# Kernel tuning notes

Measured on AMD Instinct MI355X. Metric: run time of the kernel, lower is better.

The kernel has to match this reference:

```python
import jax, jax.numpy as jnp
import numpy as np

B = 2048          # batch_size
W = 512           # input_window_size (token feature dim)
E = 16            # n_routed_experts
K = 2             # n_activated_experts (topk)
INTER = 1024      # moe_inter_dim
SH_INTER = 2 * 1024  # n_shared_experts * inter_dim
OUT = 128         # output_window_size
ROUTE_SCALE = 1.0


def setup_inputs() -> dict:
    key = jax.random.key(0)
    ks = jax.random.split(key, 18)
    sW = 1.0 / np.sqrt(W)
    sI = 1.0 / np.sqrt(INTER)
    sS = 1.0 / np.sqrt(SH_INTER)
    return {
        "x": jax.random.normal(ks[0], (B, W), jnp.float32),
        "task_id": 0,
        # gate: F.linear(x, weight) -> no bias used in forward
        "gate_w": jax.random.normal(ks[1], (E, W), jnp.float32) * sW,
        # routed experts, stacked over E. torch Linear: y = x @ w.T + b
        "w1": jax.random.normal(ks[2], (E, INTER, W), jnp.float32) * sW,
        "b1": jax.random.normal(ks[3], (E, INTER), jnp.float32) * sW,
        "w2": jax.random.normal(ks[4], (E, W, INTER), jnp.float32) * sI,
        "b2": jax.random.normal(ks[5], (E, W), jnp.float32) * sI,
        "w3": jax.random.normal(ks[6], (E, INTER, W), jnp.float32) * sW,
        "b3": jax.random.normal(ks[7], (E, INTER), jnp.float32) * sW,
        # shared expert (SwiGLU-like MLP on the window dim)
        "sw1": jax.random.normal(ks[8], (SH_INTER, W), jnp.float32) * sW,
        "sb1": jax.random.normal(ks[9], (SH_INTER,), jnp.float32) * sW,
        "sw2": jax.random.normal(ks[10], (W, SH_INTER), jnp.float32) * sS,
        "sb2": jax.random.normal(ks[11], (W,), jnp.float32) * sS,
        "sw3": jax.random.normal(ks[12], (SH_INTER, W), jnp.float32) * sW,
        "sb3": jax.random.normal(ks[13], (SH_INTER,), jnp.float32) * sW,
        # output layer
        "ow": jax.random.normal(ks[14], (OUT, W), jnp.float32) * sW,
        "ob": jax.random.normal(ks[15], (OUT,), jnp.float32) * sW,
    }


def reference(x, task_id, gate_w, w1, b1, w2, b2, w3, b3,
              sw1, sb1, sw2, sb2, sw3, sb3, ow, ob):
    xf = x.reshape(x.shape[0], -1)                      # [B, W]
    b = xf.shape[0]

    # --- gate: softmax scores, top-k routing weights ---
    scores = jax.nn.softmax(xf @ gate_w.T, axis=-1)     # [B, E] (fp32 softmax)
    top_w, top_i = jax.lax.top_k(scores, K)             # [B, K]
    top_w = (top_w * ROUTE_SCALE).astype(xf.dtype)
    # dense combine weights: zero except selected experts (topk indices distinct)
    combine = jnp.zeros((b, E), xf.dtype).at[jnp.arange(b)[:, None], top_i].add(top_w)

    # --- routed experts (dense, all experts on all tokens, masked combine) ---
    h1 = jnp.einsum('bw,eiw->bei', xf, w1) + b1          # [B, E, INTER]
    h3 = jnp.einsum('bw,eiw->bei', xf, w3) + b3
    h = jax.nn.leaky_relu(h1) * h3                       # leaky_relu slope 0.01
    eo = jnp.einsum('bei,ewi->bew', h, w2) + b2          # [B, E, W]
    y = jnp.einsum('bew,be->bw', eo, combine)            # weighted combine

    # --- shared expert ---
    z = (jax.nn.leaky_relu(xf @ sw1.T + sb1) * (xf @ sw3.T + sb3)) @ sw2.T + sb2

    out = (y + z) @ ow.T + ob                            # [B, OUT]
    return out.reshape(B, OUT)
```

## Files before the change

kernel.cpp:

```cpp
#include <hip/hip_runtime.h>

#define B_TOK 2048
#define W_DIM 512
#define E_N 16
#define INTER 1024
#define SH_INTER 2048
#define OUT_DIM 128

typedef unsigned short u16;
typedef unsigned int u32;
typedef __attribute__((ext_vector_type(8))) short bf16x8;
typedef __attribute__((ext_vector_type(4))) float f32x4;

#define WAITV(N) asm volatile("s_waitcnt vmcnt(" #N ")" ::: "memory")
#define WAITL()  asm volatile("s_waitcnt lgkmcnt(0)" ::: "memory")
#define SBAR()   __builtin_amdgcn_s_barrier()

__device__ __forceinline__ u16 f2b(float f) {
    union { float f; unsigned u; } x; x.f = f;
    unsigned r = x.u + 0x7FFFu + ((x.u >> 16) & 1u);
    return (u16)(r >> 16);
}

__device__ __forceinline__ u32 cvtpk(float lo, float hi) {
    u32 r;
    asm("v_cvt_pk_bf16_f32 %0, %1, %2" : "=v"(r) : "v"(lo), "v"(hi));
    return r;
}

__device__ __forceinline__ void gld16(const void* g, void* l) {
    __builtin_amdgcn_global_load_lds(
        (const __attribute__((address_space(1))) void*)g,
        (__attribute__((address_space(3))) void*)l, 16, 0, 0);
}


struct CastSeg { const float4* src; uint4* dst; int n8; };
struct CastArgs { CastSeg s[2]; };

__global__ __launch_bounds__(256)
void cast_small(CastArgs a) {
    int rem = blockIdx.x * 2048;
    int s = 0;
    while (rem >= a.s[s].n8) { rem -= a.s[s].n8; ++s; }
    const float4* __restrict__ src = a.s[s].src + (size_t)rem * 2;
    uint4* __restrict__ dst = a.s[s].dst + rem;
    const int t = threadIdx.x;
    #pragma unroll
    for (int k = 0; k < 8; ++k) {
        float4 v0 = src[(size_t)(t + k * 256) * 2];
        float4 v1 = src[(size_t)(t + k * 256) * 2 + 1];
        uint4 o;
        o.x = cvtpk(v0.x, v0.y);
        o.y = cvtpk(v0.z, v0.w);
        o.z = cvtpk(v1.x, v1.y);
        o.w = cvtpk(v1.z, v1.w);
        dst[t + k * 256] = o;
    }
}

__global__ __launch_bounds__(256)
void gate_topk(const float* __restrict__ x, const float* __restrict__ gw,
               int* __restrict__ topi, float* __restrict__ topw) {
    const int lane = threadIdx.x & 63;
    const int wv   = threadIdx.x >> 6;
    const int t    = blockIdx.x * 4 + wv;
    const int e = lane >> 2, q = lane & 3;
    const float4* xr = (const float4*)(x + (size_t)t * W_DIM);
    const float4* wr = (const float4*)(gw + (size_t)e * W_DIM);
    float s = 0.f;
    #pragma unroll
    for (int i = 0; i < W_DIM / 16; ++i) {
        float4 a = xr[q + 4 * i];
        float4 b = wr[q + 4 * i];
        s += a.x * b.x + a.y * b.y + a.z * b.z + a.w * b.w;
    }
    s += __shfl_xor(s, 1);
    s += __shfl_xor(s, 2);
    float sc[16];
    #pragma unroll
    for (int ee = 0; ee < 16; ++ee) sc[ee] = __shfl(s, ee * 4);
    float mx = sc[0];
    #pragma unroll
    for (int ee = 1; ee < 16; ++ee) mx = fmaxf(mx, sc[ee]);
    float p[16]; float sum = 0.f;
    #pragma unroll
    for (int ee = 0; ee < 16; ++ee) { p[ee] = expf(sc[ee] - mx); sum += p[ee]; }
    const float inv = 1.f / sum;
    int i0 = 0; float v0 = sc[0];
    #pragma unroll
    for (int ee = 1; ee < 16; ++ee) if (sc[ee] > v0) { v0 = sc[ee]; i0 = ee; }
    int i1 = -1; float v1 = -1e30f;
    #pragma unroll
    for (int ee = 0; ee < 16; ++ee) if (ee != i0 && sc[ee] > v1) { v1 = sc[ee]; i1 = ee; }
    if (lane == 0) {
        topi[t * 2 + 0] = i0; topi[t * 2 + 1] = i1;
        topw[t * 2 + 0] = p[i0] * inv; topw[t * 2 + 1] = p[i1] * inv;
    }
}

__global__ __launch_bounds__(256)
void route_build(const int* __restrict__ topi, const float* __restrict__ topw,
                 int* __restrict__ meta, int* __restrict__ glist,
                 float* __restrict__ job_w, int* __restrict__ t2r) {
    __shared__ int cnt[16], cur[16], offs[16];
    const int tid = threadIdx.x;
    if (tid < 16) { cnt[tid] = 0; cur[tid] = 0; }
    __syncthreads();
    for (int i = tid; i < 2 * B_TOK; i += 256) atomicAdd(&cnt[topi[i]], 1);
    __syncthreads();
    if (tid == 0) {
        int acc = 0, jc = 0;
        for (int e = 0; e < 16; ++e) {
            offs[e] = acc; meta[e] = cnt[e]; meta[32 + e] = acc; acc += cnt[e];
        }
        for (int e = 0; e < 16; ++e)
            for (int m = 0; m < cnt[e]; m += 128) { meta[64 + jc] = e; meta[128 + jc] = m; ++jc; }
        for (int m = 0; m < B_TOK; m += 128) { meta[64 + jc] = 16; meta[128 + jc] = m; ++jc; }
        meta[50] = jc;
        jc = 0;
        for (int e = 0; e < 16; ++e)
            for (int m = 0; m < cnt[e]; m += 64) { meta[192 + jc] = e; meta[304 + jc] = m; ++jc; }
        for (int m = 0; m < B_TOK; m += 64) { meta[192 + jc] = 16; meta[304 + jc] = m; ++jc; }
        meta[51] = jc;
    }
    __syncthreads();
    for (int i = tid; i < 2 * B_TOK; i += 256) {
        int e = topi[i];
        int pos = atomicAdd(&cur[e], 1);
        int row = offs[e] + pos;
        glist[row] = i >> 1;
        job_w[row] = topw[i];
        t2r[i] = row;
    }
    for (int t = tid; t < B_TOK; t += 256) glist[4096 + t] = t;
}

struct BReg { float4 a1, b1, a3, b3; };

__global__ __launch_bounds__(256)
void g1_dual(const u16* __restrict__ xb, const int* __restrict__ glist, const int* __restrict__ meta,
             const float* __restrict__ w1, const float* __restrict__ w3,
             const float* __restrict__ b1, const float* __restrict__ b3,
             const float* __restrict__ sw1, const float* __restrict__ sw3,
             const float* __restrict__ sb1, const float* __restrict__ sb3,
             u16* __restrict__ hbuf, u16* __restrict__ pbuf) {
    const int job = blockIdx.x;
    if (job >= meta[50]) return;
    const int e  = meta[64 + job];
    const int m0 = meta[128 + job];
    const bool sh = (e == 16);
    if (!sh && blockIdx.y >= (INTER / 64)) return;
    const int n0 = blockIdx.y * 64;
    const int N  = sh ? SH_INTER : INTER;
    const float* B1 = sh ? sw1 : (w1 + (size_t)e * INTER * W_DIM);
    const float* B3 = sh ? sw3 : (w3 + (size_t)e * INTER * W_DIM);
    const float* bb1 = sh ? sb1 : (b1 + (size_t)e * INTER);
    const float* bb3 = sh ? sb3 : (b3 + (size_t)e * INTER);
    const int abase = sh ? (4096 + m0) : (meta[32 + e] + m0);
    const int Mrows = (sh ? B_TOK : meta[e]) - m0;
    u16* outp = sh ? pbuf : hbuf;
    const int orow0 = sh ? m0 : (meta[32 + e] + m0);

    __shared__ __align__(16) u16 lds[2 * 8192];

    const int tid = threadIdx.x, lane = tid & 63, wv = tid >> 6;
    const int rA0 = tid >> 2, rA1 = rA0 + 64;
    const int kq = (tid & 3) * 8;
    const int tok0 = glist[abase + (rA0 < Mrows ? rA0 : Mrows - 1)];
    const int tok1 = glist[abase + (rA1 < Mrows ? rA1 : Mrows - 1)];
    const u16* gA0 = xb + (size_t)tok0 * W_DIM + kq;
    const u16* gA1 = xb + (size_t)tok1 * W_DIM + kq;
    const float* gB1 = B1 + (size_t)(n0 + rA0) * W_DIM + kq;
    const float* gB3 = B3 + (size_t)(n0 + rA0) * W_DIM + kq;

    const int wm = wv >> 1, wn = wv & 1;
    const int l15 = lane & 15, lhi = lane >> 4;

    f32x4 a1[4][2] = {};
    f32x4 a3[4][2] = {};

    BReg r0, r1;

    auto loadB = [&](BReg& r, int k0) {
        r.a1 = *(const float4*)(gB1 + k0);
        r.b1 = *(const float4*)(gB1 + k0 + 4);
        r.a3 = *(const float4*)(gB3 + k0);
        r.b3 = *(const float4*)(gB3 + k0 + 4);
    };
    auto writeB = [&](const BReg& r, u16* buf) {
        uint4 o1, o3;
        o1.x = cvtpk(r.a1.x, r.a1.y); o1.y = cvtpk(r.a1.z, r.a1.w);
        o1.z = cvtpk(r.b1.x, r.b1.y); o1.w = cvtpk(r.b1.z, r.b1.w);
        o3.x = cvtpk(r.a3.x, r.a3.y); o3.y = cvtpk(r.a3.z, r.a3.w);
        o3.z = cvtpk(r.b3.x, r.b3.y); o3.w = cvtpk(r.b3.z, r.b3.w);
        *(uint4*)(buf + 4096 + tid * 8) = o1;
        *(uint4*)(buf + 6144 + tid * 8) = o3;
    };
    auto stageA = [&](u16* buf, int k0) {
        gld16(gA0 + k0, buf + tid * 8);
        gld16(gA1 + k0, buf + 2048 + tid * 8);
    };

    const int NT = W_DIM / 32;
    int cur = 0;

    stageA(lds, 0);
    loadB(r0, 0);
    WAITV(0);
    writeB(r0, lds);
    loadB(r1, 32);
    WAITL();
    SBAR();

    auto step = [&](int t, BReg& rcons, BReg& rfill) {
        u16* bufc = lds + cur * 8192;
        u16* bufn = lds + (cur ^ 1) * 8192;
        if (t + 1 < NT) stageA(bufn, (t + 1) * 32);
        if (t + 2 < NT) loadB(rfill, (t + 2) * 32);
        bf16x8 af[4], f1[2], f3[2];
        #pragma unroll
        for (int i = 0; i < 4; ++i)
            af[i] = *(const bf16x8*)&bufc[(wm * 64 + i * 16 + l15) * 32 + lhi * 8];
        #pragma unroll
        for (int j = 0; j < 2; ++j) {
            f1[j] = *(const bf16x8*)&bufc[4096 + (wn * 32 + j * 16 + l15) * 32 + lhi * 8];
            f3[j] = *(const bf16x8*)&bufc[6144 + (wn * 32 + j * 16 + l15) * 32 + lhi * 8];
        }
        if (t + 1 < NT) {
            if (t + 2 < NT) { WAITV(6); } else { WAITV(2); }
            writeB(rcons, bufn);
        }
        #pragma unroll
        for (int i = 0; i < 4; ++i)
            #pragma unroll
            for (int j = 0; j < 2; ++j) {
                a1[i][j] = __builtin_amdgcn_mfma_f32_16x16x32_bf16(af[i], f1[j], a1[i][j], 0, 0, 0);
                a3[i][j] = __builtin_amdgcn_mfma_f32_16x16x32_bf16(af[i], f3[j], a3[i][j], 0, 0, 0);
            }
        if (t + 2 < NT) { WAITV(4); } else { WAITV(0); }
        WAITL();
        SBAR();
        cur ^= 1;
    };

    for (int t = 0; t < NT; t += 2) { step(t, r1, r0); step(t + 1, r0, r1); }

    #pragma unroll
    for (int i = 0; i < 4; ++i)
    #pragma unroll
    for (int j = 0; j < 2; ++j) {
        const int col = n0 + wn * 32 + j * 16 + l15;
        const float vb1 = bb1[col];
        const float vb3 = bb3[col];
        #pragma unroll
        for (int r = 0; r < 4; ++r) {
            const int gm = wm * 64 + i * 16 + lhi * 4 + r;
            if (gm < Mrows) {
                float v1 = a1[i][j][r] + vb1;
                float v3 = a3[i][j][r] + vb3;
                v1 = v1 >= 0.f ? v1 : 0.01f * v1;
                outp[(size_t)(orow0 + gm) * N + col] = f2b(v1 * v3);
            }
        }
    }
}

struct BReg2 { float4 a, b; };

__global__ __launch_bounds__(256)
void g2_gemm(const int* __restrict__ meta,
             const u16* __restrict__ hbuf, const u16* __restrict__ pbuf,
             const float* __restrict__ w2, const float* __restrict__ b2,
             const float* __restrict__ sw2, const float* __restrict__ sb2,
             const float* __restrict__ job_w,
             float* __restrict__ y2, float* __restrict__ zbuf) {
    const int job = blockIdx.x;
    if (job >= meta[51]) return;
    const int e  = meta[192 + job];
    const int m0 = meta[304 + job];
    const bool sh = (e == 16);
    const int n0 = blockIdx.y * 64;
    const int K  = sh ? SH_INTER : INTER;
    const u16* A = sh ? pbuf : hbuf;
    const int Arow0 = sh ? m0 : (meta[32 + e] + m0);
    const float* Bw = sh ? sw2 : (w2 + (size_t)e * W_DIM * INTER);
    const float* bias = sh ? sb2 : (b2 + (size_t)e * W_DIM);
    const int Mrows = (sh ? B_TOK : meta[e]) - m0;
    const float* scale = sh ? nullptr : (job_w + Arow0);
    float* outp = sh ? zbuf : y2;

    __shared__ __align__(16) u16 lds[2 * 4096];

    const int tid = threadIdx.x, lane = tid & 63, wv = tid >> 6;
    const int rA = tid >> 2;
    const int kq = (tid & 3) * 8;
    const u16*   gA = A + (size_t)(Arow0 + (rA < Mrows ? rA : Mrows - 1)) * K + kq;
    const float* gB = Bw + (size_t)(n0 + rA) * K + kq;

    const int wm = wv >> 1, wn = wv & 1;
    const int l15 = lane & 15, lhi = lane >> 4;

    f32x4 acc[2][2] = {};

    BReg2 r0, r1;
    auto loadB = [&](BReg2& r, int k0) {
        r.a = *(const float4*)(gB + k0);
        r.b = *(const float4*)(gB + k0 + 4);
    };
    auto writeB = [&](const BReg2& r, u16* buf) {
        uint4 o;
        o.x = cvtpk(r.a.x, r.a.y); o.y = cvtpk(r.a.z, r.a.w);
        o.z = cvtpk(r.b.x, r.b.y); o.w = cvtpk(r.b.z, r.b.w);
        *(uint4*)(buf + 2048 + tid * 8) = o;
    };
    auto stageA = [&](u16* buf, int k0) { gld16(gA + k0, buf + tid * 8); };

    const int NT = K / 32;
    int cur = 0;

    stageA(lds, 0);
    loadB(r0, 0);
    WAITV(0);
    writeB(r0, lds);
    loadB(r1, 32);
    WAITL();
    SBAR();

    auto step = [&](int t, BReg2& rcons, BReg2& rfill) {
        u16* bufc = lds + cur * 4096;
        u16* bufn = lds + (cur ^ 1) * 4096;
        if (t + 1 < NT) stageA(bufn, (t + 1) * 32);
        if (t + 2 < NT) loadB(rfill, (t + 2) * 32);
        bf16x8 af[2], bf[2];
        #pragma unroll
        for (int i = 0; i < 2; ++i)
            af[i] = *(const bf16x8*)&bufc[(wm * 32 + i * 16 + l15) * 32 + lhi * 8];
        #pragma unroll
        for (int j = 0; j < 2; ++j)
            bf[j] = *(const bf16x8*)&bufc[2048 + (wn * 32 + j * 16 + l15) * 32 + lhi * 8];
        if (t + 1 < NT) {
            if (t + 2 < NT) { WAITV(3); } else { WAITV(1); }
            writeB(rcons, bufn);
        }
        #pragma unroll
        for (int i = 0; i < 2; ++i)
            #pragma unroll
            for (int j = 0; j < 2; ++j)
                acc[i][j] = __builtin_amdgcn_mfma_f32_16x16x32_bf16(af[i], bf[j], acc[i][j], 0, 0, 0);
        if (t + 2 < NT) { WAITV(2); } else { WAITV(0); }
        WAITL();
        SBAR();
        cur ^= 1;
    };

    for (int t = 0; t < NT; t += 2) { step(t, r1, r0); step(t + 1, r0, r1); }

    #pragma unroll
    for (int i = 0; i < 2; ++i)
    #pragma unroll
    for (int j = 0; j < 2; ++j) {
        const int col = n0 + wn * 32 + j * 16 + l15;
        const float bb = bias[col];
        #pragma unroll
        for (int r = 0; r < 4; ++r) {
            const int gm = wm * 32 + i * 16 + lhi * 4 + r;
            if (gm < Mrows) {
                float v = acc[i][j][r] + bb;
                if (scale) v *= scale[gm];
                outp[(size_t)(Arow0 + gm) * W_DIM + col] = v;
            }
        }
    }
}

__global__ __launch_bounds__(256)
void combine_k(const float* __restrict__ y2, const float* __restrict__ z,
               const int* __restrict__ t2r, u16* __restrict__ ybf) {
    int idx = blockIdx.x * 256 + threadIdx.x;
    int t = idx >> 7;
    int w4 = (idx & 127) << 2;
    int r0 = t2r[t * 2 + 0], r1 = t2r[t * 2 + 1];
    const float4 a = *(const float4*)(y2 + (size_t)r0 * W_DIM + w4);
    const float4 b = *(const float4*)(y2 + (size_t)r1 * W_DIM + w4);
    const float4 c = *(const float4*)(z + (size_t)t * W_DIM + w4);
    ushort4 o;
    o.x = f2b(a.x + b.x + c.x);
    o.y = f2b(a.y + b.y + c.y);
    o.z = f2b(a.z + b.z + c.z);
    o.w = f2b(a.w + b.w + c.w);
    *(ushort4*)(ybf + (size_t)t * W_DIM + w4) = o;
}

__global__ __launch_bounds__(256)
void gout(const u16* __restrict__ ybf, const u16* __restrict__ owb,
          const float* __restrict__ ob, float* __restrict__ out) {
    const int m0 = blockIdx.x * 64, n0 = blockIdx.y * 64;
    __shared__ __align__(16) u16 lds[2 * 4096];
    const int tid = threadIdx.x, lane = tid & 63, wv = tid >> 6;
    const int rA = tid >> 2;
    const int kq = (tid & 3) * 8;
    const u16* gA = ybf + (size_t)(m0 + rA) * W_DIM + kq;
    const u16* gB = owb + (size_t)(n0 + rA) * W_DIM + kq;
    const int wm = wv >> 1, wn = wv & 1;
    const int l15 = lane & 15, lhi = lane >> 4;
    f32x4 acc[2][2] = {};
    auto stage = [&](int s, int k0) {
        u16* b = &lds[s * 4096];
        gld16(gA + k0, b + tid * 8);
        gld16(gB + k0, b + 2048 + tid * 8);
    };
    const int NT = W_DIM / 32;
    int cur = 0;
    stage(0, 0);
    for (int t = 0; t < NT; ++t) {
        __syncthreads();
        if (t + 1 < NT) stage(cur ^ 1, (t + 1) * 32);
        const u16* bb = &lds[cur * 4096];
        bf16x8 af[2], bf[2];
        #pragma unroll
        for (int i = 0; i < 2; ++i)
            af[i] = *(const bf16x8*)&bb[(wm * 32 + i * 16 + l15) * 32 + lhi * 8];
        #pragma unroll
        for (int j = 0; j < 2; ++j)
            bf[j] = *(const bf16x8*)&bb[2048 + (wn * 32 + j * 16 + l15) * 32 + lhi * 8];
        #pragma unroll
        for (int i = 0; i < 2; ++i)
            #pragma unroll
            for (int j = 0; j < 2; ++j)
                acc[i][j] = __builtin_amdgcn_mfma_f32_16x16x32_bf16(af[i], bf[j], acc[i][j], 0, 0, 0);
        cur ^= 1;
    }
    #pragma unroll
    for (int i = 0; i < 2; ++i)
    #pragma unroll
    for (int j = 0; j < 2; ++j) {
        const int col = n0 + wn * 32 + j * 16 + l15;
        if (col < OUT_DIM) {
            const float bb = ob[col];
            #pragma unroll
            for (int r = 0; r < 4; ++r) {
                const int gm = wm * 32 + i * 16 + lhi * 4 + r;
                out[(size_t)(m0 + gm) * OUT_DIM + col] = acc[i][j][r] + bb;
            }
        }
    }
}

extern "C" void kernel_launch(void* const* d_in, const int* in_sizes, int n_in,
                              void* d_out, int out_size, void* d_ws, size_t ws_size,
                              hipStream_t stream) {
    const float* x      = (const float*)d_in[0];
    const float* gate_w = (const float*)d_in[2];
    const float* w1     = (const float*)d_in[3];
    const float* b1     = (const float*)d_in[4];
    const float* w2     = (const float*)d_in[5];
    const float* b2     = (const float*)d_in[6];
    const float* w3     = (const float*)d_in[7];
    const float* b3     = (const float*)d_in[8];
    const float* sw1    = (const float*)d_in[9];
    const float* sb1    = (const float*)d_in[10];
    const float* sw2    = (const float*)d_in[11];
    const float* sb2    = (const float*)d_in[12];
    const float* sw3    = (const float*)d_in[13];
    const float* sb3    = (const float*)d_in[14];
    const float* ow     = (const float*)d_in[15];
    const float* ob     = (const float*)d_in[16];
    float* out = (float*)d_out;

    char* ws = (char*)d_ws;
    size_t off = 0;
    auto alloc = [&](size_t bytes) -> void* {
        void* p = (void*)(ws + off);
        off += (bytes + 255) & ~(size_t)255;
        return p;
    };

    int*   meta   = (int*)alloc(2048);
    int*   topi   = (int*)alloc((size_t)B_TOK * 2 * 4);
    float* topw   = (float*)alloc((size_t)B_TOK * 2 * 4);
    int*   t2r    = (int*)alloc((size_t)B_TOK * 2 * 4);
    int*   glist  = (int*)alloc((size_t)(B_TOK * 2 + B_TOK) * 4);
    float* job_w  = (float*)alloc((size_t)B_TOK * 2 * 4);
    u16*   xb     = (u16*)alloc((size_t)B_TOK * W_DIM * 2);
    u16*   owb    = (u16*)alloc((size_t)OUT_DIM * W_DIM * 2);
    u16*   hbuf   = (u16*)alloc((size_t)B_TOK * 2 * INTER * 2);
    u16*   pbuf   = (u16*)alloc((size_t)B_TOK * SH_INTER * 2);
    float* y2     = (float*)alloc((size_t)B_TOK * 2 * W_DIM * 4);
    float* zbuf   = (float*)alloc((size_t)B_TOK * W_DIM * 4);
    u16*   ybf    = (u16*)alloc((size_t)B_TOK * W_DIM * 2);
    if (off > ws_size) return;

    dim3 blk(256);

    CastArgs ca;
    ca.s[0] = { (const float4*)x,  (uint4*)xb,  B_TOK * W_DIM / 8 };
    ca.s[1] = { (const float4*)ow, (uint4*)owb, OUT_DIM * W_DIM / 8 };
    const int total8 = B_TOK * W_DIM / 8 + OUT_DIM * W_DIM / 8;
    cast_small<<<dim3(total8 / 2048), blk, 0, stream>>>(ca);

    gate_topk<<<dim3(B_TOK / 4), blk, 0, stream>>>(x, gate_w, topi, topw);
    route_build<<<1, blk, 0, stream>>>(topi, topw, meta, glist, job_w, t2r);

    g1_dual<<<dim3(64, SH_INTER / 64), blk, 0, stream>>>(
        xb, glist, meta, w1, w3, b1, b3, sw1, sw3, sb1, sb3, hbuf, pbuf);

    g2_gemm<<<dim3(112, W_DIM / 64), blk, 0, stream>>>(
        meta, hbuf, pbuf, w2, b2, sw2, sb2, job_w, y2, zbuf);

    combine_k<<<dim3(B_TOK * W_DIM / 4 / 256), blk, 0, stream>>>(y2, zbuf, t2r, ybf);

    gout<<<dim3(B_TOK / 64, 2), blk, 0, stream>>>(ybf, owb, ob, out);
}
```

Measured before the change: 140.0 us.

## Triple-buffer GEMM tiles with direct-to-LDS fp32 weight loads and XOR swizzle

Both expert GEMM kernels replace the register-staged, double-buffered weight path with a three-stage LDS ring. Every stage, including the fp32 weight tiles, is filled with direct global-to-LDS loads. Weights stay fp32 in LDS and are converted to bf16 when read into fragments, and the A and B tiles use XOR swizzles to avoid bank conflicts. This is meant to deepen prefetch and cut the register round trip for weights, but it doubles the LDS footprint per stage, which may lower occupancy, and it moves conversion work into the inner loop.

After: 147.5 us. +5.3%, slower.

```diff
diff --git a/kernel.cpp b/kernel.cpp
--- a/kernel.cpp
+++ b/kernel.cpp
@@ -136,8 +136,6 @@
     for (int t = tid; t < B_TOK; t += 256) glist[4096 + t] = t;
 }
 
-struct BReg { float4 a1, b1, a3, b3; };
-
 __global__ __launch_bounds__(256)
 void g1_dual(const u16* __restrict__ xb, const int* __restrict__ glist, const int* __restrict__ meta,
              const float* __restrict__ w1, const float* __restrict__ w3,
@@ -162,17 +160,21 @@
     u16* outp = sh ? pbuf : hbuf;
     const int orow0 = sh ? m0 : (meta[32 + e] + m0);
 
-    __shared__ __align__(16) u16 lds[2 * 8192];
+    __shared__ __align__(16) u16 lds[3 * 12288];
 
     const int tid = threadIdx.x, lane = tid & 63, wv = tid >> 6;
     const int rA0 = tid >> 2, rA1 = rA0 + 64;
-    const int kq = (tid & 3) * 8;
+    const int kqA = ((tid & 3) ^ ((tid >> 3) & 3)) * 8;
     const int tok0 = glist[abase + (rA0 < Mrows ? rA0 : Mrows - 1)];
     const int tok1 = glist[abase + (rA1 < Mrows ? rA1 : Mrows - 1)];
-    const u16* gA0 = xb + (size_t)tok0 * W_DIM + kq;
-    const u16* gA1 = xb + (size_t)tok1 * W_DIM + kq;
-    const float* gB1 = B1 + (size_t)(n0 + rA0) * W_DIM + kq;
-    const float* gB3 = B3 + (size_t)(n0 + rA0) * W_DIM + kq;
+    const u16* gA0 = xb + (size_t)tok0 * W_DIM + kqA;
+    const u16* gA1 = xb + (size_t)tok1 * W_DIM + kqA;
+    const int rB0 = tid >> 3;
+    const int lslot = (tid & 7) ^ (rB0 & 7);
+    const float* gB1_0 = B1 + (size_t)(n0 + rB0) * W_DIM + lslot * 4;
+    const float* gB1_1 = gB1_0 + (size_t)32 * W_DIM;
+    const float* gB3_0 = B3 + (size_t)(n0 + rB0) * W_DIM + lslot * 4;
+    const float* gB3_1 = gB3_0 + (size_t)32 * W_DIM;
 
     const int wm = wv >> 1, wn = wv & 1;
     const int l15 = lane & 15, lhi = lane >> 4;
@@ -180,57 +182,54 @@
     f32x4 a1[4][2] = {};
     f32x4 a3[4][2] = {};
 
-    BReg r0, r1;
-
-    auto loadB = [&](BReg& r, int k0) {
-        r.a1 = *(const float4*)(gB1 + k0);
-        r.b1 = *(const float4*)(gB1 + k0 + 4);
-        r.a3 = *(const float4*)(gB3 + k0);
-        r.b3 = *(const float4*)(gB3 + k0 + 4);
-    };
-    auto writeB = [&](const BReg& r, u16* buf) {
-        uint4 o1, o3;
-        o1.x = cvtpk(r.a1.x, r.a1.y); o1.y = cvtpk(r.a1.z, r.a1.w);
-        o1.z = cvtpk(r.b1.x, r.b1.y); o1.w = cvtpk(r.b1.z, r.b1.w);
-        o3.x = cvtpk(r.a3.x, r.a3.y); o3.y = cvtpk(r.a3.z, r.a3.w);
-        o3.z = cvtpk(r.b3.x, r.b3.y); o3.w = cvtpk(r.b3.z, r.b3.w);
-        *(uint4*)(buf + 4096 + tid * 8) = o1;
-        *(uint4*)(buf + 6144 + tid * 8) = o3;
-    };
-    auto stageA = [&](u16* buf, int k0) {
-        gld16(gA0 + k0, buf + tid * 8);
-        gld16(gA1 + k0, buf + 2048 + tid * 8);
+    auto stage = [&](int s, int kt) {
+        u16* b = &lds[s * 12288];
+        gld16(gA0 + kt * 32, b + tid * 8);
+        gld16(gA1 + kt * 32, b + 2048 + tid * 8);
+        gld16(gB1_0 + kt * 32, b + 4096 + tid * 8);
+        gld16(gB1_1 + kt * 32, b + 6144 + tid * 8);
+        gld16(gB3_0 + kt * 32, b + 8192 + tid * 8);
+        gld16(gB3_1 + kt * 32, b + 10240 + tid * 8);
+    };
+
+    auto ldA = [&](const u16* Ab, int r) -> bf16x8 {
+        const int p = lhi ^ ((r >> 1) & 3);
+        return *(const bf16x8*)&Ab[r * 32 + p * 8];
+    };
+    auto ldB = [&](const float* Bf, int r) -> bf16x8 {
+        const int s0 = (lhi * 2) ^ (r & 7);
+        const float4 lo = *(const float4*)(Bf + r * 32 + s0 * 4);
+        const float4 hi = *(const float4*)(Bf + r * 32 + (s0 ^ 1) * 4);
+        union { u32 u[4]; bf16x8 v; } o;
+        o.u[0] = cvtpk(lo.x, lo.y); o.u[1] = cvtpk(lo.z, lo.w);
+        o.u[2] = cvtpk(hi.x, hi.y); o.u[3] = cvtpk(hi.z, hi.w);
+        return o.v;
     };
 
     const int NT = W_DIM / 32;
+    stage(0, 0); stage(1, 1); stage(2, 2);
+
     int cur = 0;
-
-    stageA(lds, 0);
-    loadB(r0, 0);
-    WAITV(0);
-    writeB(r0, lds);
-    loadB(r1, 32);
-    WAITL();
-    SBAR();
-
-    auto step = [&](int t, BReg& rcons, BReg& rfill) {
-        u16* bufc = lds + cur * 8192;
-        u16* bufn = lds + (cur ^ 1) * 8192;
-        if (t + 1 < NT) stageA(bufn, (t + 1) * 32);
-        if (t + 2 < NT) loadB(rfill, (t + 2) * 32);
+    for (int t = 0; t < NT; ++t) {
+        if (t + 2 < NT)      { WAITV(12); }
+        else if (t + 1 < NT) { WAITV(6); }
+        else                 { WAITV(0); }
+        SBAR();
+        const u16* bb = &lds[cur * 12288];
+        const float* Bf1 = (const float*)&bb[4096];
+        const float* Bf3 = (const float*)&bb[8192];
         bf16x8 af[4], f1[2], f3[2];
         #pragma unroll
         for (int i = 0; i < 4; ++i)
-            af[i] = *(const bf16x8*)&bufc[(wm * 64 + i * 16 + l15) * 32 + lhi * 8];
+            af[i] = ldA(bb, wm * 64 + i * 16 + l15);
         #pragma unroll
         for (int j = 0; j < 2; ++j) {
-            f1[j] = *(const bf16x8*)&bufc[4096 + (wn * 32 + j * 16 + l15) * 32 + lhi * 8];
-            f3[j] = *(const bf16x8*)&bufc[6144 + (wn * 32 + j * 16 + l15) * 32 + lhi * 8];
+            f1[j] = ldB(Bf1, wn * 32 + j * 16 + l15);
+            f3[j] = ldB(Bf3, wn * 32 + j * 16 + l15);
         }
-        if (t + 1 < NT) {
-            if (t + 2 < NT) { WAITV(6); } else { WAITV(2); }
-            writeB(rcons, bufn);
-        }
+        WAITL();
+        SBAR();
+        if (t + 3 < NT) stage(cur, t + 3);
         #pragma unroll
         for (int i = 0; i < 4; ++i)
             #pragma unroll
@@ -238,13 +237,8 @@
                 a1[i][j] = __builtin_amdgcn_mfma_f32_16x16x32_bf16(af[i], f1[j], a1[i][j], 0, 0, 0);
                 a3[i][j] = __builtin_amdgcn_mfma_f32_16x16x32_bf16(af[i], f3[j], a3[i][j], 0, 0, 0);
             }
-        if (t + 2 < NT) { WAITV(4); } else { WAITV(0); }
-        WAITL();
-        SBAR();
-        cur ^= 1;
-    };
-
-    for (int t = 0; t < NT; t += 2) { step(t, r1, r0); step(t + 1, r0, r1); }
+        cur = (cur == 2) ? 0 : cur + 1;
+    }
 
     #pragma unroll
     for (int i = 0; i < 4; ++i)
@@ -265,8 +259,6 @@
         }
     }
 }
-
-struct BReg2 { float4 a, b; };
 
 __global__ __launch_bounds__(256)
 void g2_gemm(const int* __restrict__ meta,
@@ -290,71 +282,70 @@
     const float* scale = sh ? nullptr : (job_w + Arow0);
     float* outp = sh ? zbuf : y2;
 
-    __shared__ __align__(16) u16 lds[2 * 4096];
+    __shared__ __align__(16) u16 lds[3 * 6144];
 
     const int tid = threadIdx.x, lane = tid & 63, wv = tid >> 6;
     const int rA = tid >> 2;
-    const int kq = (tid & 3) * 8;
-    const u16*   gA = A + (size_t)(Arow0 + (rA < Mrows ? rA : Mrows - 1)) * K + kq;
-    const float* gB = Bw + (size_t)(n0 + rA) * K + kq;
+    const int kqA = ((tid & 3) ^ ((tid >> 3) & 3)) * 8;
+    const u16* gA = A + (size_t)(Arow0 + (rA < Mrows ? rA : Mrows - 1)) * K + kqA;
+    const int rB0 = tid >> 3;
+    const int lslot = (tid & 7) ^ (rB0 & 7);
+    const float* gB0 = Bw + (size_t)(n0 + rB0) * K + lslot * 4;
+    const float* gB1p = gB0 + (size_t)32 * K;
 
     const int wm = wv >> 1, wn = wv & 1;
     const int l15 = lane & 15, lhi = lane >> 4;
 
     f32x4 acc[2][2] = {};
 
-    BReg2 r0, r1;
-    auto loadB = [&](BReg2& r, int k0) {
-        r.a = *(const float4*)(gB + k0);
-        r.b = *(const float4*)(gB + k0 + 4);
-    };
-    auto writeB = [&](const BReg2& r, u16* buf) {
-        uint4 o;
-        o.x = cvtpk(r.a.x, r.a.y); o.y = cvtpk(r.a.z, r.a.w);
-        o.z = cvtpk(r.b.x, r.b.y); o.w = cvtpk(r.b.z, r.b.w);
-        *(uint4*)(buf + 2048 + tid * 8) = o;
-    };
-    auto stageA = [&](u16* buf, int k0) { gld16(gA + k0, buf + tid * 8); };
+    auto stage = [&](int s, int kt) {
+        u16* b = &lds[s * 6144];
+        gld16(gA + kt * 32, b + tid * 8);
+        gld16(gB0 + kt * 32, b + 2048 + tid * 8);
+        gld16(gB1p + kt * 32, b + 4096 + tid * 8);
+    };
+    auto ldA = [&](const u16* Ab, int r) -> bf16x8 {
+        const int p = lhi ^ ((r >> 1) & 3);
+        return *(const bf16x8*)&Ab[r * 32 + p * 8];
+    };
+    auto ldB = [&](const float* Bf, int r) -> bf16x8 {
+        const int s0 = (lhi * 2) ^ (r & 7);
+        const float4 lo = *(const float4*)(Bf + r * 32 + s0 * 4);
+        const float4 hi = *(const float4*)(Bf + r * 32 + (s0 ^ 1) * 4);
+        union { u32 u[4]; bf16x8 v; } o;
+        o.u[0] = cvtpk(lo.x, lo.y); o.u[1] = cvtpk(lo.z, lo.w);
+        o.u[2] = cvtpk(hi.x, hi.y); o.u[3] = cvtpk(hi.z, hi.w);
+        return o.v;
+    };
 
     const int NT = K / 32;
+    stage(0, 0); stage(1, 1); stage(2, 2);
+
     int cur = 0;
-
-    stageA(lds, 0);
-    loadB(r0, 0);
-    WAITV(0);
-    writeB(r0, lds);
-    loadB(r1, 32);
-    WAITL();
-    SBAR();
-
-    auto step = [&](int t, BReg2& rcons, BReg2& rfill) {
-        u16* bufc = lds + cur * 4096;
-        u16* bufn = lds + (cur ^ 1) * 4096;
-        if (t + 1 < NT) stageA(bufn, (t + 1) * 32);
-        if (t + 2 < NT) loadB(rfill, (t + 2) * 32);
+    for (int t = 0; t < NT; ++t) {
+        if (t + 2 < NT)      { WAITV(6); }
+        else if (t + 1 < NT) { WAITV(3); }
+        else                 { WAITV(0); }
+        SBAR();
+        const u16* bb = &lds[cur * 6144];
+        const float* Bf = (const float*)&bb[2048];
         bf16x8 af[2], bf[2];
         #pragma unroll
         for (int i = 0; i < 2; ++i)
-            af[i] = *(const bf16x8*)&bufc[(wm * 32 + i * 16 + l15) * 32 + lhi * 8];
+            af[i] = ldA(bb, wm * 32 + i * 16 + l15);
         #pragma unroll
         for (int j = 0; j < 2; ++j)
-            bf[j] = *(const bf16x8*)&bufc[2048 + (wn * 32 + j * 16 + l15) * 32 + lhi * 8];
-        if (t + 1 < NT) {
-            if (t + 2 < NT) { WAITV(3); } else { WAITV(1); }
-            writeB(rcons, bufn);
-        }
+            bf[j] = ldB(Bf, wn * 32 + j * 16 + l15);
+        WAITL();
+        SBAR();
+        if (t + 3 < NT) stage(cur, t + 3);
         #pragma unroll
         for (int i = 0; i < 2; ++i)
             #pragma unroll
             for (int j = 0; j < 2; ++j)
                 acc[i][j] = __builtin_amdgcn_mfma_f32_16x16x32_bf16(af[i], bf[j], acc[i][j], 0, 0, 0);
-        if (t + 2 < NT) { WAITV(2); } else { WAITV(0); }
-        WAITL();
-        SBAR();
-        cur ^= 1;
-    };
-
-    for (int t = 0; t < NT; t += 2) { step(t, r1, r0); step(t + 1, r0, r1); }
+        cur = (cur == 2) ? 0 : cur + 1;
+    }
 
     #pragma unroll
     for (int i = 0; i < 2; ++i)
```
